# Optimization experiments

Measured on AMD Instinct MI355X. Metric: run time of the kernel, lower is better.

The kernel has to match this reference:

```python
import jax, jax.numpy as jnp
import numpy as np

N = 8192
E = 131072
D_IN = 128
D_OUT = 128
EPS = 1e-5


def setup_inputs() -> dict:
    key = jax.random.key(0)
    k1, k2, k3, k4 = jax.random.split(key, 4)
    x = jax.random.normal(k1, (N, D_IN), dtype=jnp.float32)
    edge_index = jax.random.randint(k2, (2, E), 0, N, dtype=jnp.int64)
    weight = jax.random.normal(k3, (D_IN, D_OUT), dtype=jnp.float32)
    bias = jax.random.normal(k4, (D_OUT,), dtype=jnp.float32)
    return {"x": x, "edge_index": edge_index, "weight": weight, "bias": bias}


def reference(x, edge_index, weight, bias):
    n = x.shape[0]
    row, col = edge_index[0], edge_index[1]
    # dense adjacency build, exactly as the torch module does
    adj = jnp.zeros((n, n), dtype=x.dtype).at[row, col].set(1.0)
    adj = jnp.maximum(adj, adj.T)                      # symmetrize
    adj = adj + jnp.eye(n, dtype=x.dtype)              # self-loops (added, may yield 2 on diag)
    d_inv_sqrt = 1.0 / jnp.sqrt(adj.sum(axis=1) + EPS)  # [N]
    # D^{-1/2} A D^{-1/2} via broadcasting (same math as diag matmuls)
    norm_adj = d_inv_sqrt[:, None] * adj * d_inv_sqrt[None, :]
    out = norm_adj @ x            # [N, D_IN] aggregation
    out = out @ weight + bias     # [N, D_OUT]
    return out
```

## Files before the change

### kernel.cpp

```cpp
#include <hip/hip_runtime.h>
#include <stdint.h>

#define N_NODES 8192
#define NE      131072
#define DCH     128
#define WPR     256
#define MAXC    128
#define EPS     1e-5f

__global__ __launch_bounds__(256) void build_gemm_kernel(
    const void*  __restrict__ ei_raw,
    const float* __restrict__ X,
    const float* __restrict__ W,
    uint32_t* __restrict__ bm,
    int*      __restrict__ cnt,
    uint16_t* __restrict__ nbr,
    float*    __restrict__ z)
{
    int t = threadIdx.x;
    if (blockIdx.x < 512) {
        int lane = t & 63;
        const long long* p64 = (const long long*)ei_raw;
        const int*       p32 = (const int*)ei_raw;
        bool is64 = __all((unsigned long long)p64[lane] < (unsigned long long)N_NODES);
        int e = blockIdx.x * 256 + t;
        int r, c;
        if (is64) { r = (int)p64[e]; c = (int)p64[NE + e]; }
        else      { r = p32[e];      c = p32[NE + e]; }
        uint32_t mc = 1u << (c & 31), mr = 1u << (r & 31);
        uint32_t o1 = atomicOr(&bm[r * WPR + (c >> 5)], mc);
        if (!(o1 & mc)) {
            int pos = atomicAdd(&cnt[r], 1);
            if (pos < MAXC) nbr[(size_t)r * MAXC + pos] = (uint16_t)c;
        }
        uint32_t o2 = atomicOr(&bm[c * WPR + (r >> 5)], mr);
        if (!(o2 & mr)) {
            int pos = atomicAdd(&cnt[c], 1);
            if (pos < MAXC) nbr[(size_t)c * MAXC + pos] = (uint16_t)r;
        }
    } else {
        __shared__ float sA[64][132];
        int bx = blockIdx.x - 512;
        int row0 = (bx >> 1) * 64;
        int col0 = (bx & 1) * 64;
        {
            int k4 = t & 31;
            int r  = t >> 5;
            #pragma unroll
            for (int p = 0; p < 8; ++p) {
                float4 v = *(const float4*)&X[(size_t)(row0 + r + p * 8) * DCH + k4 * 4];
                *(float4*)&sA[r + p * 8][k4 * 4] = v;
            }
        }
        __syncthreads();
        int tx = t & 15, ty = t >> 4;
        int cg = col0 + tx * 4;
        int r0 = ty * 4;
        float acc[4][4] = {};
        #pragma unroll 4
        for (int k = 0; k < DCH; ++k) {
            float4 w = *(const float4*)&W[(size_t)k * DCH + cg];
            float a0 = sA[r0 + 0][k];
            float a1 = sA[r0 + 1][k];
            float a2 = sA[r0 + 2][k];
            float a3 = sA[r0 + 3][k];
            acc[0][0] += a0 * w.x; acc[0][1] += a0 * w.y; acc[0][2] += a0 * w.z; acc[0][3] += a0 * w.w;
            acc[1][0] += a1 * w.x; acc[1][1] += a1 * w.y; acc[1][2] += a1 * w.z; acc[1][3] += a1 * w.w;
            acc[2][0] += a2 * w.x; acc[2][1] += a2 * w.y; acc[2][2] += a2 * w.z; acc[2][3] += a2 * w.w;
            acc[3][0] += a3 * w.x; acc[3][1] += a3 * w.y; acc[3][2] += a3 * w.z; acc[3][3] += a3 * w.w;
        }
        #pragma unroll
        for (int i = 0; i < 4; ++i) {
            float4 o;
            o.x = acc[i][0]; o.y = acc[i][1]; o.z = acc[i][2]; o.w = acc[i][3];
            *(float4*)&z[(size_t)(row0 + r0 + i) * DCH + cg] = o;
        }
    }
}

__global__ __launch_bounds__(256) void aggregate_kernel(
    const uint16_t* __restrict__ nbr,
    const int*   __restrict__ cnt,
    const float* __restrict__ z,
    const float* __restrict__ bias,
    float*       __restrict__ out)
{
    __shared__ uint32_t s_list[4][64];
    int w    = threadIdx.x >> 6;
    int lane = threadIdx.x & 63;
    int node = blockIdx.x * 4 + w;

    s_list[w][lane] = ((const uint32_t*)nbr)[(size_t)node * (MAXC / 2) + lane];
    const uint16_t* sl = (const uint16_t*)s_list[w];

    int total = __builtin_amdgcn_readfirstlane(cnt[node]);
    int cap   = total > MAXC ? MAXC : total;
    int full  = cap & ~7;
    float dn  = 1.0f / sqrtf((float)total + 1.0f + EPS);

    const float2* z2 = (const float2*)z;
    float2 self = z2[(size_t)node * 64 + lane];
    float2 a0, a1 = {0,0}, a2 = {0,0}, a3 = {0,0}, a4 = {0,0}, a5 = {0,0}, a6 = {0,0}, a7 = {0,0};
    a0.x = dn * self.x; a0.y = dn * self.y;

    for (int k = 0; k < full; k += 8) {
        #define STEPU(i, AX) {                                                \
            int j = __builtin_amdgcn_readfirstlane((int)sl[k + i]);           \
            float dj = 1.0f / sqrtf((float)cnt[j] + 1.0f + EPS);              \
            float2 q = z2[(size_t)j * 64 + lane];                             \
            AX.x += dj * q.x; AX.y += dj * q.y; }
        STEPU(0, a0) STEPU(1, a1) STEPU(2, a2) STEPU(3, a3)
        STEPU(4, a4) STEPU(5, a5) STEPU(6, a6) STEPU(7, a7)
        #undef STEPU
    }
    if (full < cap) {
        #define STEPP(i, AX) {                                                \
            int idx = full + i;                                               \
            int j = __builtin_amdgcn_readfirstlane((int)sl[idx]);             \
            bool val = idx < cap;                                             \
            j = val ? j : node;                                               \
            float dj = val ? 1.0f / sqrtf((float)cnt[j] + 1.0f + EPS) : 0.0f; \
            float2 q = z2[(size_t)j * 64 + lane];                             \
            AX.x += dj * q.x; AX.y += dj * q.y; }
        STEPP(0, a0) STEPP(1, a1) STEPP(2, a2) STEPP(3, a3)
        STEPP(4, a4) STEPP(5, a5) STEPP(6, a6) STEPP(7, a7)
        #undef STEPP
    }

    float2 bb = ((const float2*)bias)[lane];
    float2 r;
    r.x = dn * (((a0.x + a1.x) + (a2.x + a3.x)) + ((a4.x + a5.x) + (a6.x + a7.x))) + bb.x;
    r.y = dn * (((a0.y + a1.y) + (a2.y + a3.y)) + ((a4.y + a5.y) + (a6.y + a7.y))) + bb.y;
    ((float2*)out)[(size_t)node * 64 + lane] = r;
}

extern "C" void kernel_launch(void* const* d_in, const int* in_sizes, int n_in,
                              void* d_out, int out_size, void* d_ws, size_t ws_size,
                              hipStream_t stream) {
    const float* xp  = (const float*)d_in[0];
    const void*  eip = d_in[1];
    const float* Wp  = (const float*)d_in[2];
    const float* bp  = (const float*)d_in[3];
    float*       op  = (float*)d_out;

    uint8_t* ws = (uint8_t*)d_ws;
    uint32_t* bmp  = (uint32_t*)ws;
    int*      cntp = (int*)     (ws + (size_t)8 * 1024 * 1024);
    uint16_t* nbrp = (uint16_t*)(ws + (size_t)8 * 1024 * 1024 + 32 * 1024);
    float*    zp   = (float*)   (ws + (size_t)10 * 1024 * 1024 + 32 * 1024);

    hipMemsetAsync(bmp, 0, (size_t)8 * 1024 * 1024 + 32 * 1024, stream);
    build_gemm_kernel<<<768, 256, 0, stream>>>(eip, xp, Wp, bmp, cntp, nbrp, zp);
    aggregate_kernel<<<N_NODES / 4, 256, 0, stream>>>(nbrp, cntp, zp, bp, op);
}
```

Measured before the change: 119.3 us.

## Pre-scale projected rows by inverse-sqrt degree and pad neighbor lists to zero row

Adds a finish kernel that computes each node's inverse-sqrt degree once, writes a pre-scaled copy of the projected features, and pads each neighbor list to a multiple of eight with an index pointing at an all-zero row. The aggregation loop then only gathers and adds rows, with no per-neighbor count load or sqrt and no predicated tail loop. The cost is an extra kernel launch and an extra full read and write of the feature matrix.

Result: faster. 112.3 us (-5.8%).

```diff
diff --git a/kernel.cpp b/kernel.cpp
--- a/kernel.cpp
+++ b/kernel.cpp
@@ -6,6 +6,7 @@
 #define DCH     128
 #define WPR     256
 #define MAXC    128
+#define ZROW    8192
 #define EPS     1e-5f
 
 __global__ __launch_bounds__(256) void build_gemm_kernel(
@@ -78,10 +79,40 @@
     }
 }
 
+__global__ __launch_bounds__(256) void finish_kernel(
+    const int*   __restrict__ cnt,
+    uint16_t*    __restrict__ nbr,
+    const float* __restrict__ z,
+    float*       __restrict__ y,
+    float*       __restrict__ dinv)
+{
+    int w    = threadIdx.x >> 6;
+    int lane = threadIdx.x & 63;
+    int node = blockIdx.x * 4 + w;
+
+    int total = __builtin_amdgcn_readfirstlane(cnt[node]);
+    int cap   = total > MAXC ? MAXC : total;
+    int kpad  = (cap + 7) & ~7;
+    float dn  = 1.0f / sqrtf((float)total + 1.0f + EPS);
+
+    if (lane == 0) dinv[node] = dn;
+    if (lane < 8 && cap + lane < kpad)
+        nbr[(size_t)node * MAXC + cap + lane] = (uint16_t)ZROW;
+
+    const float2* z2 = (const float2*)z;
+    float2*       y2 = (float2*)y;
+    float2 v = z2[(size_t)node * 64 + lane];
+    float2 s; s.x = dn * v.x; s.y = dn * v.y;
+    y2[(size_t)node * 64 + lane] = s;
+
+    if (node == 0) { float2 zz = {0.0f, 0.0f}; y2[(size_t)ZROW * 64 + lane] = zz; }
+}
+
 __global__ __launch_bounds__(256) void aggregate_kernel(
     const uint16_t* __restrict__ nbr,
     const int*   __restrict__ cnt,
-    const float* __restrict__ z,
+    const float* __restrict__ dinv,
+    const float* __restrict__ y,
     const float* __restrict__ bias,
     float*       __restrict__ out)
 {
@@ -95,36 +126,21 @@
 
     int total = __builtin_amdgcn_readfirstlane(cnt[node]);
     int cap   = total > MAXC ? MAXC : total;
-    int full  = cap & ~7;
-    float dn  = 1.0f / sqrtf((float)total + 1.0f + EPS);
+    int kpad  = (cap + 7) & ~7;
+    float dn  = dinv[node];
 
-    const float2* z2 = (const float2*)z;
-    float2 self = z2[(size_t)node * 64 + lane];
-    float2 a0, a1 = {0,0}, a2 = {0,0}, a3 = {0,0}, a4 = {0,0}, a5 = {0,0}, a6 = {0,0}, a7 = {0,0};
-    a0.x = dn * self.x; a0.y = dn * self.y;
+    const float2* y2 = (const float2*)y;
+    float2 a0 = y2[(size_t)node * 64 + lane];
+    float2 a1 = {0,0}, a2 = {0,0}, a3 = {0,0}, a4 = {0,0}, a5 = {0,0}, a6 = {0,0}, a7 = {0,0};
 
-    for (int k = 0; k < full; k += 8) {
-        #define STEPU(i, AX) {                                                \
-            int j = __builtin_amdgcn_readfirstlane((int)sl[k + i]);           \
-            float dj = 1.0f / sqrtf((float)cnt[j] + 1.0f + EPS);              \
-            float2 q = z2[(size_t)j * 64 + lane];                             \
-            AX.x += dj * q.x; AX.y += dj * q.y; }
+    for (int k = 0; k < kpad; k += 8) {
+        #define STEPU(i, AX) {                                      \
+            int j = __builtin_amdgcn_readfirstlane((int)sl[k + i]); \
+            float2 q = y2[(size_t)j * 64 + lane];                   \
+            AX.x += q.x; AX.y += q.y; }
         STEPU(0, a0) STEPU(1, a1) STEPU(2, a2) STEPU(3, a3)
         STEPU(4, a4) STEPU(5, a5) STEPU(6, a6) STEPU(7, a7)
         #undef STEPU
-    }
-    if (full < cap) {
-        #define STEPP(i, AX) {                                                \
-            int idx = full + i;                                               \
-            int j = __builtin_amdgcn_readfirstlane((int)sl[idx]);             \
-            bool val = idx < cap;                                             \
-            j = val ? j : node;                                               \
-            float dj = val ? 1.0f / sqrtf((float)cnt[j] + 1.0f + EPS) : 0.0f; \
-            float2 q = z2[(size_t)j * 64 + lane];                             \
-            AX.x += dj * q.x; AX.y += dj * q.y; }
-        STEPP(0, a0) STEPP(1, a1) STEPP(2, a2) STEPP(3, a3)
-        STEPP(4, a4) STEPP(5, a5) STEPP(6, a6) STEPP(7, a7)
-        #undef STEPP
     }
 
     float2 bb = ((const float2*)bias)[lane];
@@ -144,12 +160,15 @@
     float*       op  = (float*)d_out;
 
     uint8_t* ws = (uint8_t*)d_ws;
-    uint32_t* bmp  = (uint32_t*)ws;
-    int*      cntp = (int*)     (ws + (size_t)8 * 1024 * 1024);
-    uint16_t* nbrp = (uint16_t*)(ws + (size_t)8 * 1024 * 1024 + 32 * 1024);
-    float*    zp   = (float*)   (ws + (size_t)10 * 1024 * 1024 + 32 * 1024);
+    uint32_t* bmp   = (uint32_t*)ws;
+    int*      cntp  = (int*)     (ws + 8388608);
+    uint16_t* nbrp  = (uint16_t*)(ws + 8421376);
+    float*    zp    = (float*)   (ws + 10518528);
+    float*    yp    = (float*)   (ws + 14712832);
+    float*    dinvp = (float*)   (ws + 18907648);
 
-    hipMemsetAsync(bmp, 0, (size_t)8 * 1024 * 1024 + 32 * 1024, stream);
+    hipMemsetAsync(bmp, 0, 8388608 + 32768, stream);
     build_gemm_kernel<<<768, 256, 0, stream>>>(eip, xp, Wp, bmp, cntp, nbrp, zp);
-    aggregate_kernel<<<N_NODES / 4, 256, 0, stream>>>(nbrp, cntp, zp, bp, op);
+    finish_kernel<<<N_NODES / 4, 256, 0, stream>>>(cntp, nbrp, zp, yp, dinvp);
+    aggregate_kernel<<<N_NODES / 4, 256, 0, stream>>>(nbrp, cntp, dinvp, yp, bp, op);
 }
```
